# Kernel optimization log

Measured on AMD Instinct MI355X. Metric: run time of the kernel, lower is better.

The kernel has to match this reference:

```python
import jax, jax.numpy as jnp
import numpy as np

BATCH = 4096
DIM = 256
TEMP = 0.5
COS_EPS = 1e-8  # torch.nn.CosineSimilarity default eps


def setup_inputs() -> dict:
    key = jax.random.key(0)
    k1, k2 = jax.random.split(key)
    zis = jax.random.normal(k1, (BATCH, DIM), dtype=jnp.float32)
    zjs = jax.random.normal(k2, (BATCH, DIM), dtype=jnp.float32)
    return {"zis": zis, "zjs": zjs}


def reference(zis, zjs):
    n = zis.shape[0]  # batch_size
    # representations = cat([zjs, zis]) -> (2N, D)
    reps = jnp.concatenate([zjs, zis], axis=0)
    # cosine similarity matrix: dot / max(|x||y|, eps)  (matches torch CosineSimilarity)
    norms = jnp.linalg.norm(reps, axis=-1)  # (2N,)
    sim = (reps @ reps.T) / jnp.maximum(norms[:, None] * norms[None, :], COS_EPS)  # (2N, 2N)
    # positives: diag at offset +N (rows 0..N-1) then offset -N (rows N..2N-1)
    pos = jnp.concatenate([jnp.diagonal(sim, n), jnp.diagonal(sim, -n)])  # (2N,)
    # CE with label 0 over [pos, negatives]: negatives = row minus {diag, positive};
    # logsumexp([pos] + negatives) == logsumexp(row with only the self-diagonal masked),
    # since the positive appears exactly once in the row.
    two_n = 2 * n
    logits = sim / TEMP
    logits = jnp.where(jnp.eye(two_n, dtype=bool), -jnp.inf, logits)
    lse = jax.nn.logsumexp(logits, axis=-1)  # (2N,)
    loss = jnp.sum(lse - pos / TEMP)  # CrossEntropyLoss(reduction='sum')
    return loss / two_n
```

## Files before the change

### kernel.cpp

```cpp
#include <hip/hip_runtime.h>
#include <hip/hip_bf16.h>

#define TWO_N  8192
#define N_HALF 4096
#define DIMS   256

typedef __bf16 bf16x8 __attribute__((ext_vector_type(8)));
typedef float  f32x4  __attribute__((ext_vector_type(4)));
typedef unsigned short ushort8v __attribute__((ext_vector_type(8)));

__device__ __forceinline__ float fast_exp2(float x) {
#if __has_builtin(__builtin_amdgcn_exp2f)
    return __builtin_amdgcn_exp2f(x);
#else
    float r; asm("v_exp_f32 %0, %1" : "=v"(r) : "v"(x)); return r;
#endif
}

#define GLOAD_LDS16(g, l)                                                      \
    __builtin_amdgcn_global_load_lds(                                          \
        (const __attribute__((address_space(1))) unsigned int*)(g),            \
        (__attribute__((address_space(3))) unsigned int*)(l), 16, 0, 0)

__global__ __launch_bounds__(256) void nrm_kernel(const float* __restrict__ zis,
                                                  const float* __restrict__ zjs,
                                                  unsigned short* __restrict__ swz,
                                                  float* __restrict__ out)
{
    if (blockIdx.x == 0 && threadIdx.x == 0) out[0] = 0.f;

    const int tid = threadIdx.x;
    const int l32 = tid & 31;
    const int row = blockIdx.x * 8 + (tid >> 5);
    const int k0  = l32 * 8;

    const float* src = (row < N_HALF) ? (zjs + (size_t)row * DIMS)
                                      : (zis + (size_t)(row - N_HALF) * DIMS);
    const float4 v0 = reinterpret_cast<const float4*>(src + k0)[0];
    const float4 v1 = reinterpret_cast<const float4*>(src + k0 + 4)[0];
    float ss = v0.x * v0.x + v0.y * v0.y + v0.z * v0.z + v0.w * v0.w
             + v1.x * v1.x + v1.y * v1.y + v1.z * v1.z + v1.w * v1.w;
#pragma unroll
    for (int m = 1; m < 32; m <<= 1) ss += __shfl_xor(ss, m, 64);
    const float inv = rsqrtf(ss) * 1.69864360045f;

    const float vals[8] = {v0.x, v0.y, v0.z, v0.w, v1.x, v1.y, v1.z, v1.w};
    ushort8v o;
#pragma unroll
    for (int j = 0; j < 8; ++j) {
        __hip_bfloat16 b = __float2bfloat16(vals[j] * inv);
        o[j] = *reinterpret_cast<unsigned short*>(&b);
    }
    const int chunk = ((row >> 4) * 8 + (l32 >> 2)) * 64 + (l32 & 3) * 16 + (row & 15);
    *reinterpret_cast<ushort8v*>(swz + (size_t)chunk * 8) = o;
}

__global__ __launch_bounds__(512) void ntx_kernel(const __bf16* __restrict__ swz,
                                                  float* __restrict__ rowsum_part,
                                                  float* __restrict__ pos_part)
{
    __shared__ __bf16 abuf[2][32768];

    const int lane = threadIdx.x & 63;
    const int wave = threadIdx.x >> 6;
    const int l15  = lane & 15;
    const int quad = lane >> 4;

    const int rg   = blockIdx.x & 15;
    const int cs   = blockIdx.x >> 4;
    const int wr0  = rg * 512 + wave * 64;
    const int p0   = wr0 ^ N_HALF;

    auto stage = [&](int buf, int c) {
        const __bf16* gsrc = swz + (size_t)(cs * 32 + c * 8 + wave) * 4096 + lane * 8;
#pragma unroll
        for (int h = 0; h < 8; ++h)
            GLOAD_LDS16(gsrc + h * 512, &abuf[buf][wave * 4096 + h * 512]);
    };

    stage(0, 0);

    bf16x8 bfrag[4][8];
#pragma unroll
    for (int t = 0; t < 4; ++t) {
        const __bf16* bp = swz + (size_t)((wr0 >> 4) + t) * 4096 + lane * 8;
#pragma unroll
        for (int kk = 0; kk < 8; ++kk)
            bfrag[t][kk] = *reinterpret_cast<const bf16x8*>(bp + kk * 512);
    }

    float sum_exp[4] = {0.f, 0.f, 0.f, 0.f};
    float pos_acc = 0.f;

    auto burst = [&](f32x4* acc, const bf16x8* af) {
#pragma unroll
        for (int t = 0; t < 4; ++t) acc[t] = f32x4{0.f, 0.f, 0.f, 0.f};
#pragma unroll
        for (int kk = 0; kk < 8; ++kk) {
#pragma unroll
            for (int t = 0; t < 4; ++t)
                acc[t] = __builtin_amdgcn_mfma_f32_16x16x32_bf16(
                    af[kk], bfrag[t][kk], acc[t], 0, 0, 0);
        }
    };

    auto drain = [&](const f32x4* acc, int c0) {
        const bool special = (c0 < wr0 + 64 && c0 + 16 > wr0) ||
                             (c0 < p0 + 64 && c0 + 16 > p0);
        if (!special) {
#pragma unroll
            for (int t = 0; t < 4; ++t)
#pragma unroll
                for (int j = 0; j < 4; ++j)
                    sum_exp[t] += fast_exp2(acc[t][j]);
        } else {
#pragma unroll
            for (int t = 0; t < 4; ++t) {
                const int r = wr0 + t * 16 + l15;
#pragma unroll
                for (int j = 0; j < 4; ++j) {
                    const int col = c0 + quad * 4 + j;
                    const float e = fast_exp2(acc[t][j]);
                    sum_exp[t] += (col == r) ? 0.f : e;
                    if (col == (r ^ N_HALF)) pos_acc += acc[t][j];
                }
            }
        }
    };

    asm volatile("s_waitcnt vmcnt(0)" ::: "memory");
    __syncthreads();

    f32x4 accE[4], accO[4];
    int pc0 = -1;

    int cur = 0;
    for (int c = 0; c < 4; ++c) {
        if (c < 3) stage(cur ^ 1, c + 1);

        const int cc_base = cs * 512 + c * 128;

        bf16x8 a0[8], a1[8];
#pragma unroll
        for (int kk = 0; kk < 8; ++kk)
            a0[kk] = *reinterpret_cast<const bf16x8*>(&abuf[cur][kk * 512 + lane * 8]);

        for (int it = 0; it < 8; it += 2) {
#pragma unroll
            for (int kk = 0; kk < 8; ++kk)
                a1[kk] = *reinterpret_cast<const bf16x8*>(
                    &abuf[cur][(it + 1) * 4096 + kk * 512 + lane * 8]);

            burst(accE, a0);
            if (pc0 >= 0) drain(accO, pc0);

            if (it + 2 < 8) {
#pragma unroll
                for (int kk = 0; kk < 8; ++kk)
                    a0[kk] = *reinterpret_cast<const bf16x8*>(
                        &abuf[cur][(it + 2) * 4096 + kk * 512 + lane * 8]);
            }

            burst(accO, a1);
            drain(accE, cc_base + it * 16);
            pc0 = cc_base + (it + 1) * 16;
        }

        asm volatile("s_waitcnt vmcnt(0)" ::: "memory");
        __syncthreads();
        cur ^= 1;
    }
    drain(accO, pc0);

#pragma unroll
    for (int t = 0; t < 4; ++t) {
        float s = sum_exp[t];
        s += __shfl_xor(s, 16, 64);
        s += __shfl_xor(s, 32, 64);
        if (lane < 16)
            rowsum_part[(size_t)cs * TWO_N + wr0 + t * 16 + lane] = s;
    }

#pragma unroll
    for (int m = 1; m < 64; m <<= 1) pos_acc += __shfl_xor(pos_acc, m, 64);
    if (lane == 0) pos_part[blockIdx.x * 8 + wave] = pos_acc;
}

__global__ __launch_bounds__(1024) void fin1_kernel(const float* __restrict__ rowsum_part,
                                                    const float* __restrict__ pos_part,
                                                    float* __restrict__ out)
{
    __shared__ float red[16];
    const int t = threadIdx.x;
    const int r = blockIdx.x * 1024 + t;
    float acc = 0.f;
#pragma unroll
    for (int cs = 0; cs < 16; ++cs)
        acc += rowsum_part[(size_t)cs * TWO_N + r];
    float v = logf(acc);
    if (r < 2048)
        v -= 0.69314718055994531f * pos_part[r];
#pragma unroll
    for (int m = 1; m < 64; m <<= 1) v += __shfl_xor(v, m, 64);
    if ((t & 63) == 0) red[t >> 6] = v;
    __syncthreads();
    if (t == 0) {
        float s = 0.f;
#pragma unroll
        for (int w = 0; w < 16; ++w) s += red[w];
        atomicAdd(out, s / (float)TWO_N);
    }
}

extern "C" void kernel_launch(void* const* d_in, const int* in_sizes, int n_in,
                              void* d_out, int out_size, void* d_ws, size_t ws_size,
                              hipStream_t stream)
{
    const float* zis = (const float*)d_in[0];
    const float* zjs = (const float*)d_in[1];

    unsigned short* swz = (unsigned short*)d_ws;
    float* rowsum_part  = (float*)((char*)d_ws + (size_t)TWO_N * DIMS * sizeof(unsigned short));
    float* pos_part     = rowsum_part + (size_t)16 * TWO_N;

    nrm_kernel<<<TWO_N / 8, 256, 0, stream>>>(zis, zjs, swz, (float*)d_out);
    ntx_kernel<<<256, 512, 0, stream>>>((const __bf16*)swz, rowsum_part, pos_part);
    fin1_kernel<<<8, 1024, 0, stream>>>(rowsum_part, pos_part, (float*)d_out);
}
```

Measured before the change: 93.13 us.

## Halve per-wave row tile and double grid to raise occupancy

Each wave now handles 32 rows instead of 64, and the block covers 256 rows with a smaller 64 KB double-buffered LDS tile streamed over 8 stages. The grid doubles to 512 blocks and launch bounds request 4 blocks per CU, which targets occupancy and latency hiding. The explicit even/odd software pipelining of MFMA bursts and exp drains is removed in favour of a simple per-tile loop. The trade-off is more LDS reads per MFMA, since the B fragment is reused across fewer rows, and the lost manual overlap of MFMA with exp work.

Measured after the change: 90.25 us. 3.1% less time.

```diff
diff --git a/kernel.cpp b/kernel.cpp
--- a/kernel.cpp
+++ b/kernel.cpp
@@ -55,125 +55,101 @@
     *reinterpret_cast<ushort8v*>(swz + (size_t)chunk * 8) = o;
 }
 
-__global__ __launch_bounds__(512) void ntx_kernel(const __bf16* __restrict__ swz,
-                                                  float* __restrict__ rowsum_part,
-                                                  float* __restrict__ pos_part)
-{
-    __shared__ __bf16 abuf[2][32768];
+__global__ __launch_bounds__(512, 4) void ntx_kernel(const __bf16* __restrict__ swz,
+                                                     float* __restrict__ rowsum_part,
+                                                     float* __restrict__ pos_part)
+{
+    __shared__ __bf16 abuf[2][16384];
 
     const int lane = threadIdx.x & 63;
     const int wave = threadIdx.x >> 6;
     const int l15  = lane & 15;
     const int quad = lane >> 4;
 
-    const int rg   = blockIdx.x & 15;
-    const int cs   = blockIdx.x >> 4;
-    const int wr0  = rg * 512 + wave * 64;
+    const int rg   = blockIdx.x & 31;
+    const int cs   = blockIdx.x >> 5;
+    const int wr0  = rg * 256 + wave * 32;
     const int p0   = wr0 ^ N_HALF;
 
     auto stage = [&](int buf, int c) {
-        const __bf16* gsrc = swz + (size_t)(cs * 32 + c * 8 + wave) * 4096 + lane * 8;
-#pragma unroll
-        for (int h = 0; h < 8; ++h)
-            GLOAD_LDS16(gsrc + h * 512, &abuf[buf][wave * 4096 + h * 512]);
+        const __bf16* gsrc = swz + (size_t)(cs * 32 + c * 4) * 4096
+                           + (wave * 4) * 512 + lane * 8;
+#pragma unroll
+        for (int h = 0; h < 4; ++h)
+            GLOAD_LDS16(gsrc + h * 512, &abuf[buf][(wave * 4 + h) * 512]);
     };
 
     stage(0, 0);
 
-    bf16x8 bfrag[4][8];
-#pragma unroll
-    for (int t = 0; t < 4; ++t) {
+    bf16x8 bfrag[2][8];
+#pragma unroll
+    for (int t = 0; t < 2; ++t) {
         const __bf16* bp = swz + (size_t)((wr0 >> 4) + t) * 4096 + lane * 8;
 #pragma unroll
         for (int kk = 0; kk < 8; ++kk)
             bfrag[t][kk] = *reinterpret_cast<const bf16x8*>(bp + kk * 512);
     }
 
-    float sum_exp[4] = {0.f, 0.f, 0.f, 0.f};
+    float sum_exp[2] = {0.f, 0.f};
     float pos_acc = 0.f;
 
-    auto burst = [&](f32x4* acc, const bf16x8* af) {
-#pragma unroll
-        for (int t = 0; t < 4; ++t) acc[t] = f32x4{0.f, 0.f, 0.f, 0.f};
-#pragma unroll
-        for (int kk = 0; kk < 8; ++kk) {
-#pragma unroll
-            for (int t = 0; t < 4; ++t)
-                acc[t] = __builtin_amdgcn_mfma_f32_16x16x32_bf16(
-                    af[kk], bfrag[t][kk], acc[t], 0, 0, 0);
-        }
-    };
-
-    auto drain = [&](const f32x4* acc, int c0) {
-        const bool special = (c0 < wr0 + 64 && c0 + 16 > wr0) ||
-                             (c0 < p0 + 64 && c0 + 16 > p0);
-        if (!special) {
-#pragma unroll
-            for (int t = 0; t < 4; ++t)
-#pragma unroll
-                for (int j = 0; j < 4; ++j)
-                    sum_exp[t] += fast_exp2(acc[t][j]);
-        } else {
-#pragma unroll
-            for (int t = 0; t < 4; ++t) {
-                const int r = wr0 + t * 16 + l15;
-#pragma unroll
-                for (int j = 0; j < 4; ++j) {
-                    const int col = c0 + quad * 4 + j;
-                    const float e = fast_exp2(acc[t][j]);
-                    sum_exp[t] += (col == r) ? 0.f : e;
-                    if (col == (r ^ N_HALF)) pos_acc += acc[t][j];
+    asm volatile("s_waitcnt vmcnt(0)" ::: "memory");
+    __syncthreads();
+
+    int cur = 0;
+    for (int c = 0; c < 8; ++c) {
+        if (c < 7) stage(cur ^ 1, c + 1);
+
+        const int cc_base = cs * 512 + c * 64;
+
+#pragma unroll
+        for (int it = 0; it < 4; ++it) {
+            bf16x8 a[8];
+#pragma unroll
+            for (int kk = 0; kk < 8; ++kk)
+                a[kk] = *reinterpret_cast<const bf16x8*>(
+                    &abuf[cur][it * 4096 + kk * 512 + lane * 8]);
+
+            f32x4 acc[2] = {{0.f, 0.f, 0.f, 0.f}, {0.f, 0.f, 0.f, 0.f}};
+#pragma unroll
+            for (int kk = 0; kk < 8; ++kk) {
+                acc[0] = __builtin_amdgcn_mfma_f32_16x16x32_bf16(
+                    a[kk], bfrag[0][kk], acc[0], 0, 0, 0);
+                acc[1] = __builtin_amdgcn_mfma_f32_16x16x32_bf16(
+                    a[kk], bfrag[1][kk], acc[1], 0, 0, 0);
+            }
+
+            const int c0 = cc_base + it * 16;
+            const bool special = (c0 < wr0 + 32 && c0 + 16 > wr0) ||
+                                 (c0 < p0 + 32 && c0 + 16 > p0);
+            if (!special) {
+#pragma unroll
+                for (int t = 0; t < 2; ++t)
+#pragma unroll
+                    for (int j = 0; j < 4; ++j)
+                        sum_exp[t] += fast_exp2(acc[t][j]);
+            } else {
+#pragma unroll
+                for (int t = 0; t < 2; ++t) {
+                    const int r = wr0 + t * 16 + l15;
+#pragma unroll
+                    for (int j = 0; j < 4; ++j) {
+                        const int col = c0 + quad * 4 + j;
+                        const float e = fast_exp2(acc[t][j]);
+                        sum_exp[t] += (col == r) ? 0.f : e;
+                        if (col == (r ^ N_HALF)) pos_acc += acc[t][j];
+                    }
                 }
             }
         }
-    };
-
-    asm volatile("s_waitcnt vmcnt(0)" ::: "memory");
-    __syncthreads();
-
-    f32x4 accE[4], accO[4];
-    int pc0 = -1;
-
-    int cur = 0;
-    for (int c = 0; c < 4; ++c) {
-        if (c < 3) stage(cur ^ 1, c + 1);
-
-        const int cc_base = cs * 512 + c * 128;
-
-        bf16x8 a0[8], a1[8];
-#pragma unroll
-        for (int kk = 0; kk < 8; ++kk)
-            a0[kk] = *reinterpret_cast<const bf16x8*>(&abuf[cur][kk * 512 + lane * 8]);
-
-        for (int it = 0; it < 8; it += 2) {
-#pragma unroll
-            for (int kk = 0; kk < 8; ++kk)
-                a1[kk] = *reinterpret_cast<const bf16x8*>(
-                    &abuf[cur][(it + 1) * 4096 + kk * 512 + lane * 8]);
-
-            burst(accE, a0);
-            if (pc0 >= 0) drain(accO, pc0);
-
-            if (it + 2 < 8) {
-#pragma unroll
-                for (int kk = 0; kk < 8; ++kk)
-                    a0[kk] = *reinterpret_cast<const bf16x8*>(
-                        &abuf[cur][(it + 2) * 4096 + kk * 512 + lane * 8]);
-            }
-
-            burst(accO, a1);
-            drain(accE, cc_base + it * 16);
-            pc0 = cc_base + (it + 1) * 16;
-        }
 
         asm volatile("s_waitcnt vmcnt(0)" ::: "memory");
         __syncthreads();
         cur ^= 1;
     }
-    drain(accO, pc0);
-
-#pragma unroll
-    for (int t = 0; t < 4; ++t) {
+
+#pragma unroll
+    for (int t = 0; t < 2; ++t) {
         float s = sum_exp[t];
         s += __shfl_xor(s, 16, 64);
         s += __shfl_xor(s, 32, 64);
@@ -198,7 +174,7 @@
     for (int cs = 0; cs < 16; ++cs)
         acc += rowsum_part[(size_t)cs * TWO_N + r];
     float v = logf(acc);
-    if (r < 2048)
+    if (r < 4096)
         v -= 0.69314718055994531f * pos_part[r];
 #pragma unroll
     for (int m = 1; m < 64; m <<= 1) v += __shfl_xor(v, m, 64);
@@ -224,6 +200,6 @@
     float* pos_part     = rowsum_part + (size_t)16 * TWO_N;
 
     nrm_kernel<<<TWO_N / 8, 256, 0, stream>>>(zis, zjs, swz, (float*)d_out);
-    ntx_kernel<<<256, 512, 0, stream>>>((const __bf16*)swz, rowsum_part, pos_part);
+    ntx_kernel<<<512, 512, 0, stream>>>((const __bf16*)swz, rowsum_part, pos_part);
     fin1_kernel<<<8, 1024, 0, stream>>>(rowsum_part, pos_part, (float*)d_out);
 }
```

## Switch similarity GEMM from bf16 to fp8 MFMA with doubled grid split

Applied to the files above, without the earlier changes.

Normalized rows are now quantized to fp8 (e4m3 via cvt_pk_fp8) instead of bf16, and the similarity tiles use the 16x16x32 fp8 MFMA. This halves the workspace and LDS footprint and targets the higher fp8 matrix throughput. The column split doubles to 32 slices over 512 blocks, with occupancy hinted via launch_bounds(512,4), and the explicit even/odd burst–drain software pipeline is replaced by a simpler unrolled loop. The cost is precision: fp8 has far less mantissa than bf16, so the logsumexp loss may drift further from the reference.

New measurement: 87.56 us. 6.0% less time.

```diff
diff --git a/kernel.cpp b/kernel.cpp
--- a/kernel.cpp
+++ b/kernel.cpp
@@ -5,9 +5,7 @@
 #define N_HALF 4096
 #define DIMS   256
 
-typedef __bf16 bf16x8 __attribute__((ext_vector_type(8)));
-typedef float  f32x4  __attribute__((ext_vector_type(4)));
-typedef unsigned short ushort8v __attribute__((ext_vector_type(8)));
+typedef float f32x4 __attribute__((ext_vector_type(4)));
 
 __device__ __forceinline__ float fast_exp2(float x) {
 #if __has_builtin(__builtin_amdgcn_exp2f)
@@ -24,7 +22,7 @@
 
 __global__ __launch_bounds__(256) void nrm_kernel(const float* __restrict__ zis,
                                                   const float* __restrict__ zjs,
-                                                  unsigned short* __restrict__ swz,
+                                                  unsigned char* __restrict__ swz,
                                                   float* __restrict__ out)
 {
     if (blockIdx.x == 0 && threadIdx.x == 0) out[0] = 0.f;
@@ -44,22 +42,23 @@
     for (int m = 1; m < 32; m <<= 1) ss += __shfl_xor(ss, m, 64);
     const float inv = rsqrtf(ss) * 1.69864360045f;
 
-    const float vals[8] = {v0.x, v0.y, v0.z, v0.w, v1.x, v1.y, v1.z, v1.w};
-    ushort8v o;
-#pragma unroll
-    for (int j = 0; j < 8; ++j) {
-        __hip_bfloat16 b = __float2bfloat16(vals[j] * inv);
-        o[j] = *reinterpret_cast<unsigned short*>(&b);
-    }
-    const int chunk = ((row >> 4) * 8 + (l32 >> 2)) * 64 + (l32 & 3) * 16 + (row & 15);
-    *reinterpret_cast<ushort8v*>(swz + (size_t)chunk * 8) = o;
-}
-
-__global__ __launch_bounds__(512) void ntx_kernel(const __bf16* __restrict__ swz,
-                                                  float* __restrict__ rowsum_part,
-                                                  float* __restrict__ pos_part)
-{
-    __shared__ __bf16 abuf[2][32768];
+    int w0 = 0, w1 = 0;
+    w0 = __builtin_amdgcn_cvt_pk_fp8_f32(v0.x * inv, v0.y * inv, w0, 0);
+    w0 = __builtin_amdgcn_cvt_pk_fp8_f32(v0.z * inv, v0.w * inv, w0, 1);
+    w1 = __builtin_amdgcn_cvt_pk_fp8_f32(v1.x * inv, v1.y * inv, w1, 0);
+    w1 = __builtin_amdgcn_cvt_pk_fp8_f32(v1.z * inv, v1.w * inv, w1, 1);
+
+    const size_t byte = ((size_t)((row >> 4) * 8 + (l32 >> 2)) * 64
+                         + (l32 & 3) * 16 + (row & 15)) * 8;
+    int2 o; o.x = w0; o.y = w1;
+    *reinterpret_cast<int2*>(swz + byte) = o;
+}
+
+__global__ __launch_bounds__(512, 4) void ntx_kernel(const unsigned char* __restrict__ swz,
+                                                     float* __restrict__ rowsum_part,
+                                                     float* __restrict__ pos_part)
+{
+    __shared__ unsigned char abuf[2][16384];
 
     const int lane = threadIdx.x & 63;
     const int wave = threadIdx.x >> 6;
@@ -72,105 +71,84 @@
     const int p0   = wr0 ^ N_HALF;
 
     auto stage = [&](int buf, int c) {
-        const __bf16* gsrc = swz + (size_t)(cs * 32 + c * 8 + wave) * 4096 + lane * 8;
-#pragma unroll
-        for (int h = 0; h < 8; ++h)
-            GLOAD_LDS16(gsrc + h * 512, &abuf[buf][wave * 4096 + h * 512]);
+        const unsigned char* gsrc = swz + ((size_t)(cs * 128 + c * 32)) * 512
+                                  + wave * 2048 + lane * 16;
+        GLOAD_LDS16(gsrc,       &abuf[buf][wave * 2048]);
+        GLOAD_LDS16(gsrc + 1024, &abuf[buf][wave * 2048 + 1024]);
     };
 
     stage(0, 0);
 
-    bf16x8 bfrag[4][8];
+    long long bfrag[4][8];
 #pragma unroll
     for (int t = 0; t < 4; ++t) {
-        const __bf16* bp = swz + (size_t)((wr0 >> 4) + t) * 4096 + lane * 8;
+        const unsigned char* bp = swz + (size_t)((wr0 >> 4) + t) * 4096 + lane * 8;
 #pragma unroll
         for (int kk = 0; kk < 8; ++kk)
-            bfrag[t][kk] = *reinterpret_cast<const bf16x8*>(bp + kk * 512);
+            bfrag[t][kk] = *reinterpret_cast<const long long*>(bp + kk * 512);
     }
 
     float sum_exp[4] = {0.f, 0.f, 0.f, 0.f};
     float pos_acc = 0.f;
 
-    auto burst = [&](f32x4* acc, const bf16x8* af) {
-#pragma unroll
-        for (int t = 0; t < 4; ++t) acc[t] = f32x4{0.f, 0.f, 0.f, 0.f};
-#pragma unroll
-        for (int kk = 0; kk < 8; ++kk) {
-#pragma unroll
-            for (int t = 0; t < 4; ++t)
-                acc[t] = __builtin_amdgcn_mfma_f32_16x16x32_bf16(
-                    af[kk], bfrag[t][kk], acc[t], 0, 0, 0);
-        }
-    };
-
-    auto drain = [&](const f32x4* acc, int c0) {
-        const bool special = (c0 < wr0 + 64 && c0 + 16 > wr0) ||
-                             (c0 < p0 + 64 && c0 + 16 > p0);
-        if (!special) {
-#pragma unroll
-            for (int t = 0; t < 4; ++t)
-#pragma unroll
-                for (int j = 0; j < 4; ++j)
-                    sum_exp[t] += fast_exp2(acc[t][j]);
-        } else {
-#pragma unroll
-            for (int t = 0; t < 4; ++t) {
-                const int r = wr0 + t * 16 + l15;
-#pragma unroll
-                for (int j = 0; j < 4; ++j) {
-                    const int col = c0 + quad * 4 + j;
-                    const float e = fast_exp2(acc[t][j]);
-                    sum_exp[t] += (col == r) ? 0.f : e;
-                    if (col == (r ^ N_HALF)) pos_acc += acc[t][j];
+    asm volatile("s_waitcnt vmcnt(0)" ::: "memory");
+    __syncthreads();
+
+    int cur = 0;
+    for (int c = 0; c < 4; ++c) {
+        if (c < 3) stage(cur ^ 1, c + 1);
+
+        const int cc_base = cs * 256 + c * 64;
+
+#pragma unroll
+        for (int it = 0; it < 4; ++it) {
+            const unsigned char* ab = &abuf[cur][it * 4096 + lane * 8];
+
+            f32x4 acc[4] = {{0.f, 0.f, 0.f, 0.f}, {0.f, 0.f, 0.f, 0.f},
+                            {0.f, 0.f, 0.f, 0.f}, {0.f, 0.f, 0.f, 0.f}};
+#pragma unroll
+            for (int h = 0; h < 2; ++h) {
+                long long a[4];
+#pragma unroll
+                for (int k4 = 0; k4 < 4; ++k4)
+                    a[k4] = *reinterpret_cast<const long long*>(ab + (h * 4 + k4) * 512);
+#pragma unroll
+                for (int k4 = 0; k4 < 4; ++k4) {
+#pragma unroll
+                    for (int t = 0; t < 4; ++t)
+                        acc[t] = __builtin_amdgcn_mfma_f32_16x16x32_fp8_fp8(
+                            a[k4], bfrag[t][h * 4 + k4], acc[t], 0, 0, 0);
+                }
+            }
+
+            const int c0 = cc_base + it * 16;
+            const bool special = (c0 < wr0 + 64 && c0 + 16 > wr0) ||
+                                 (c0 < p0 + 64 && c0 + 16 > p0);
+            if (!special) {
+#pragma unroll
+                for (int t = 0; t < 4; ++t)
+#pragma unroll
+                    for (int j = 0; j < 4; ++j)
+                        sum_exp[t] += fast_exp2(acc[t][j]);
+            } else {
+#pragma unroll
+                for (int t = 0; t < 4; ++t) {
+                    const int r = wr0 + t * 16 + l15;
+#pragma unroll
+                    for (int j = 0; j < 4; ++j) {
+                        const int col = c0 + quad * 4 + j;
+                        const float e = fast_exp2(acc[t][j]);
+                        sum_exp[t] += (col == r) ? 0.f : e;
+                        if (col == (r ^ N_HALF)) pos_acc += acc[t][j];
+                    }
                 }
             }
         }
-    };
-
-    asm volatile("s_waitcnt vmcnt(0)" ::: "memory");
-    __syncthreads();
-
-    f32x4 accE[4], accO[4];
-    int pc0 = -1;
-
-    int cur = 0;
-    for (int c = 0; c < 4; ++c) {
-        if (c < 3) stage(cur ^ 1, c + 1);
-
-        const int cc_base = cs * 512 + c * 128;
-
-        bf16x8 a0[8], a1[8];
-#pragma unroll
-        for (int kk = 0; kk < 8; ++kk)
-            a0[kk] = *reinterpret_cast<const bf16x8*>(&abuf[cur][kk * 512 + lane * 8]);
-
-        for (int it = 0; it < 8; it += 2) {
-#pragma unroll
-            for (int kk = 0; kk < 8; ++kk)
-                a1[kk] = *reinterpret_cast<const bf16x8*>(
-                    &abuf[cur][(it + 1) * 4096 + kk * 512 + lane * 8]);
-
-            burst(accE, a0);
-            if (pc0 >= 0) drain(accO, pc0);
-
-            if (it + 2 < 8) {
-#pragma unroll
-                for (int kk = 0; kk < 8; ++kk)
-                    a0[kk] = *reinterpret_cast<const bf16x8*>(
-                        &abuf[cur][(it + 2) * 4096 + kk * 512 + lane * 8]);
-            }
-
-            burst(accO, a1);
-            drain(accE, cc_base + it * 16);
-            pc0 = cc_base + (it + 1) * 16;
-        }
 
         asm volatile("s_waitcnt vmcnt(0)" ::: "memory");
         __syncthreads();
         cur ^= 1;
     }
-    drain(accO, pc0);
 
 #pragma unroll
     for (int t = 0; t < 4; ++t) {
@@ -195,10 +173,10 @@
     const int r = blockIdx.x * 1024 + t;
     float acc = 0.f;
 #pragma unroll
-    for (int cs = 0; cs < 16; ++cs)
+    for (int cs = 0; cs < 32; ++cs)
         acc += rowsum_part[(size_t)cs * TWO_N + r];
     float v = logf(acc);
-    if (r < 2048)
+    if (r < 4096)
         v -= 0.69314718055994531f * pos_part[r];
 #pragma unroll
     for (int m = 1; m < 64; m <<= 1) v += __shfl_xor(v, m, 64);
@@ -219,11 +197,11 @@
     const float* zis = (const float*)d_in[0];
     const float* zjs = (const float*)d_in[1];
 
-    unsigned short* swz = (unsigned short*)d_ws;
-    float* rowsum_part  = (float*)((char*)d_ws + (size_t)TWO_N * DIMS * sizeof(unsigned short));
-    float* pos_part     = rowsum_part + (size_t)16 * TWO_N;
+    unsigned char* swz = (unsigned char*)d_ws;
+    float* rowsum_part = (float*)((char*)d_ws + (size_t)TWO_N * DIMS);
+    float* pos_part    = rowsum_part + (size_t)32 * TWO_N;
 
     nrm_kernel<<<TWO_N / 8, 256, 0, stream>>>(zis, zjs, swz, (float*)d_out);
-    ntx_kernel<<<256, 512, 0, stream>>>((const __bf16*)swz, rowsum_part, pos_part);
+    ntx_kernel<<<512, 512, 0, stream>>>(swz, rowsum_part, pos_part);
     fin1_kernel<<<8, 1024, 0, stream>>>(rowsum_part, pos_part, (float*)d_out);
 }
```
